# Optimization experiments

Hardware: AMD Instinct MI355X
Metric: run time of the kernel (lower is better)

## Reference

```python
import jax, jax.numpy as jnp
import numpy as np

DIM = 256
HEADS = 4
DH = 64
B, N, H, W, G = 1, 6, 64, 64, 8
QLEN = H * W
SCALE = DH ** -0.5
EPS = 1e-5


def _ln(x, g, b):
    m = x.mean(-1, keepdims=True)
    v = ((x - m) ** 2).mean(-1, keepdims=True)
    return (x - m) / jnp.sqrt(v + EPS) * g + b


def setup_inputs() -> dict:
    key = jax.random.key(0)
    ks = jax.random.split(key, 16)
    hd = HEADS * DH
    p = lambda k, shp: 0.02 * jax.random.normal(k, shp, dtype=jnp.float32)
    inp = {
        'q': jax.random.normal(ks[0], (B, N, DIM, H, W), dtype=jnp.float32),
        'k': jax.random.normal(ks[1], (B, N, QLEN, G, DIM), dtype=jnp.float32),
        'v': jax.random.normal(ks[2], (B, N, QLEN, G, DIM), dtype=jnp.float32),
        'skip': jax.random.normal(ks[3], (B, DIM, H, W), dtype=jnp.float32),
        'mask': jax.random.randint(ks[4], (B, N, QLEN, 1), 0, 2).astype(bool),
        'ln_q_g': jnp.ones((DIM,), jnp.float32), 'ln_q_b': jnp.zeros((DIM,), jnp.float32),
        'wq': p(ks[5], (DIM, hd)), 'bq': jnp.zeros((hd,), jnp.float32),
        'ln_k_g': jnp.ones((DIM,), jnp.float32), 'ln_k_b': jnp.zeros((DIM,), jnp.float32),
        'wk': p(ks[6], (DIM, hd)), 'bk': jnp.zeros((hd,), jnp.float32),
        'ln_v_g': jnp.ones((DIM,), jnp.float32), 'ln_v_b': jnp.zeros((DIM,), jnp.float32),
        'wv': p(ks[7], (DIM, hd)), 'bv': jnp.zeros((hd,), jnp.float32),
        'w_proj': p(ks[8], (hd, DIM)), 'b_proj': jnp.zeros((DIM,), jnp.float32),
        'ln_pre_g': jnp.ones((DIM,), jnp.float32), 'ln_pre_b': jnp.zeros((DIM,), jnp.float32),
        'w_mlp1': p(ks[9], (DIM, 2 * DIM)), 'b_mlp1': jnp.zeros((2 * DIM,), jnp.float32),
        'w_mlp2': p(ks[10], (2 * DIM, DIM)), 'b_mlp2': jnp.zeros((DIM,), jnp.float32),
        'ln_post_g': jnp.ones((DIM,), jnp.float32), 'ln_post_b': jnp.zeros((DIM,), jnp.float32),
    }
    return inp


def reference(q, k, v, skip, mask,
              ln_q_g, ln_q_b, wq, bq,
              ln_k_g, ln_k_b, wk, bk,
              ln_v_g, ln_v_b, wv, bv,
              w_proj, b_proj,
              ln_pre_g, ln_pre_b,
              w_mlp1, b_mlp1, w_mlp2, b_mlp2,
              ln_post_g, ln_post_b):
    b, n, d, Hh, Ww = q.shape
    g = k.shape[-2]
    Qn = Hh * Ww
    # b n d H W -> b n (H W) d
    qx = jnp.transpose(q, (0, 1, 3, 4, 2)).reshape(b, n, Qn, d)
    qp = _ln(qx, ln_q_g, ln_q_b) @ wq + bq            # (b, n, Q, m*dh)
    kp = _ln(k, ln_k_g, ln_k_b) @ wk + bk             # (b, n, Q, g, m*dh)
    vp = _ln(v, ln_v_g, ln_v_b) @ wv + bv             # (b, n, Q, g, m*dh)
    qh = qp.reshape(b, n, Qn, HEADS, DH)
    kh = kp.reshape(b, n, Qn, g, HEADS, DH)
    # scores: (b, m, Q, n, g)
    dot = SCALE * jnp.einsum('bnqmd,bnqgmd->bmqng', qh, kh)
    mb = jnp.transpose(mask[..., 0], (0, 2, 1))[:, None, :, :, None]  # (b,1,Q,n,1)
    dot = jnp.where(mb, dot, jnp.float32(-1e9))
    att = jax.nn.softmax(dot.reshape(b, HEADS, Qn, n * g), axis=-1)
    vh = vp.reshape(b, n, Qn, g, HEADS, DH)
    vh = jnp.transpose(vh, (0, 4, 2, 1, 3, 5)).reshape(b, HEADS, Qn, n * g, DH)
    a = jnp.einsum('bmqk,bmqkd->bmqd', att, vh)       # (b, m, Q, dh)
    a = jnp.transpose(a, (0, 2, 1, 3)).reshape(b, Qn, HEADS * DH)
    z = a @ w_proj + b_proj
    z = z + jnp.transpose(skip, (0, 2, 3, 1)).reshape(b, Qn, d)
    z = _ln(z, ln_pre_g, ln_pre_b)
    h = jax.nn.gelu(z @ w_mlp1 + b_mlp1, approximate=False) @ w_mlp2 + b_mlp2
    z = _ln(z + h, ln_post_g, ln_post_b)
    return jnp.transpose(z.reshape(b, Hh, Ww, d), (0, 3, 1, 2))
```

## Files before the change

### kernel.cpp

```cpp
#include <hip/hip_runtime.h>
#include <hip/hip_bf16.h>
#include <math.h>

#define NF 6
#define QL 4096
#define SCALE 0.125f
#define EPSLN 1e-5f

typedef __bf16 bf16x8 __attribute__((ext_vector_type(8)));
typedef __bf16 bf16x4 __attribute__((ext_vector_type(4)));
typedef float  f32x4  __attribute__((ext_vector_type(4)));

#define OFF_WQT   0u
#define OFF_WKT   131072u
#define OFF_WVT   262144u
#define OFF_WPT   393216u
#define OFF_W1T   524288u
#define OFF_W2T   786432u
#define OFF_QH    1048576u
#define OFF_ATT   13631488u
#define OFF_OPART 16777216u

__device__ __forceinline__ unsigned short f2bf(float x) {
  union { float f; unsigned u; } v; v.f = x;
  unsigned r = v.u + 0x7FFFu + ((v.u >> 16) & 1u);
  return (unsigned short)(r >> 16);
}
__device__ __forceinline__ unsigned long long pack4bf(float a, float b, float c, float d) {
  unsigned d0 = (unsigned)f2bf(a) | ((unsigned)f2bf(b) << 16);
  unsigned d1 = (unsigned)f2bf(c) | ((unsigned)f2bf(d) << 16);
  return (unsigned long long)d0 | ((unsigned long long)d1 << 32);
}

__global__ void __launch_bounds__(256)
prep_kernel(const float* __restrict__ wq, const float* __restrict__ wk,
            const float* __restrict__ wv, const float* __restrict__ wp,
            const float* __restrict__ w1, const float* __restrict__ w2,
            unsigned short* __restrict__ wsu16)
{
  const int blk = blockIdx.x, t = threadIdx.x;
  const float* src; unsigned short* dst; int N, KT, ntile;
  if (blk < 64) {
    int mi = blk >> 4; ntile = blk & 15; N = 256; KT = 8;
    src = (mi == 0) ? wq : (mi == 1) ? wk : (mi == 2) ? wv : wp;
    dst = wsu16 + (size_t)mi * 65536;
  } else if (blk < 96) {
    ntile = blk - 64; N = 512; KT = 8; src = w1; dst = wsu16 + OFF_W1T / 2;
  } else {
    ntile = blk - 96; N = 256; KT = 16; src = w2; dst = wsu16 + OFF_W2T / 2;
  }
  const int lane = t & 63;
  const int lr = lane & 15, quad = lane >> 4;
  const int ncol = ntile * 16 + lr;
  for (int kt = (t >> 6); kt < KT; kt += 4) {
    unsigned v8[8];
#pragma unroll
    for (int j = 0; j < 8; ++j) {
      int krow = kt * 32 + quad * 8 + j;
      v8[j] = f2bf(src[(size_t)krow * N + ncol]);
    }
    uint4 u;
    u.x = v8[0] | (v8[1] << 16); u.y = v8[2] | (v8[3] << 16);
    u.z = v8[4] | (v8[5] << 16); u.w = v8[6] | (v8[7] << 16);
    *(uint4*)(dst + ((size_t)(ntile * KT + kt) * 512 + lane * 8)) = u;
  }
}

__global__ void __launch_bounds__(256, 4)
projq_kernel(const float* __restrict__ src,
             const float* __restrict__ lng, const float* __restrict__ lnb,
             const unsigned short* __restrict__ wTp,
             const float* __restrict__ bias,
             unsigned short* __restrict__ qh)
{
  __shared__ __align__(16) unsigned short s_x[64 * 264];
  const int t = threadIdx.x, blk = blockIdx.x;
  const int n = blk >> 6, qp0 = (blk & 63) << 6;

  {
    const int l16 = t & 15, dg = t >> 4;
    for (int it = 0; it < 16; ++it) {
      int dcol = it * 16 + dg;
      float4 x = *(const float4*)(src + ((size_t)(n * 256 + dcol)) * 4096 + qp0 + l16 * 4);
      s_x[(l16 * 4 + 0) * 264 + dcol] = f2bf(x.x);
      s_x[(l16 * 4 + 1) * 264 + dcol] = f2bf(x.y);
      s_x[(l16 * 4 + 2) * 264 + dcol] = f2bf(x.z);
      s_x[(l16 * 4 + 3) * 264 + dcol] = f2bf(x.w);
    }
  }
  __syncthreads();
  {
    const int row = t >> 2, sl = t & 3;
    float s = 0.f, s2 = 0.f;
#pragma unroll
    for (int i = 0; i < 8; ++i) {
      bf16x8 xv = *(const bf16x8*)(s_x + row * 264 + (i * 4 + sl) * 8);
#pragma unroll
      for (int j = 0; j < 8; ++j) { float f = (float)xv[j]; s += f; s2 += f * f; }
    }
    s += __shfl_xor(s, 1, 64);  s += __shfl_xor(s, 2, 64);
    s2 += __shfl_xor(s2, 1, 64); s2 += __shfl_xor(s2, 2, 64);
    float mu = s * (1.f / 256.f);
    float var = s2 * (1.f / 256.f) - mu * mu;
    float istd = rsqrtf(var + EPSLN);
#pragma unroll
    for (int i = 0; i < 8; ++i) {
      int c = (i * 4 + sl) * 8;
      bf16x8 xv = *(const bf16x8*)(s_x + row * 264 + c);
      f32x4 ga = *(const f32x4*)(lng + c), gb = *(const f32x4*)(lng + c + 4);
      f32x4 ba = *(const f32x4*)(lnb + c), bb = *(const f32x4*)(lnb + c + 4);
      uint4 u;
      u.x = (unsigned)f2bf(((float)xv[0] - mu) * istd * ga[0] + ba[0]) |
            ((unsigned)f2bf(((float)xv[1] - mu) * istd * ga[1] + ba[1]) << 16);
      u.y = (unsigned)f2bf(((float)xv[2] - mu) * istd * ga[2] + ba[2]) |
            ((unsigned)f2bf(((float)xv[3] - mu) * istd * ga[3] + ba[3]) << 16);
      u.z = (unsigned)f2bf(((float)xv[4] - mu) * istd * gb[0] + bb[0]) |
            ((unsigned)f2bf(((float)xv[5] - mu) * istd * gb[1] + bb[1]) << 16);
      u.w = (unsigned)f2bf(((float)xv[6] - mu) * istd * gb[2] + bb[2]) |
            ((unsigned)f2bf(((float)xv[7] - mu) * istd * gb[3] + bb[3]) << 16);
      *(uint4*)(s_x + row * 264 + c) = u;
    }
  }
  __syncthreads();

  const int w = t >> 6, lane = t & 63, lr = lane & 15, quad = lane >> 4;
  f32x4 acc[4][4];
  {
    f32x4 z = {0.f, 0.f, 0.f, 0.f};
#pragma unroll
    for (int a = 0; a < 4; ++a)
#pragma unroll
      for (int b = 0; b < 4; ++b) acc[a][b] = z;
  }
  for (int kt = 0; kt < 8; ++kt) {
    bf16x8 xf[4];
#pragma unroll
    for (int mt = 0; mt < 4; ++mt)
      xf[mt] = *(const bf16x8*)(s_x + (mt * 16 + lr) * 264 + kt * 32 + quad * 8);
#pragma unroll
    for (int nt = 0; nt < 4; ++nt) {
      bf16x8 wf = *(const bf16x8*)(wTp + ((size_t)((w * 4 + nt) * 8 + kt) * 512 + lane * 8));
#pragma unroll
      for (int mt = 0; mt < 4; ++mt)
        acc[nt][mt] = __builtin_amdgcn_mfma_f32_16x16x32_bf16(wf, xf[mt], acc[nt][mt], 0, 0, 0);
    }
  }
  __syncthreads();
#pragma unroll
  for (int nt = 0; nt < 4; ++nt) {
    int n0 = w * 64 + nt * 16 + quad * 4;
    f32x4 bb = *(const f32x4*)(bias + n0);
#pragma unroll
    for (int mt = 0; mt < 4; ++mt) {
      int m = mt * 16 + lr;
      f32x4 a = acc[nt][mt];
      *(unsigned long long*)(s_x + m * 264 + n0) =
          pack4bf(a[0] + bb[0], a[1] + bb[1], a[2] + bb[2], a[3] + bb[3]);
    }
  }
  __syncthreads();
  unsigned char* ob = (unsigned char*)qh + ((size_t)n * QL + qp0) * 512;
#pragma unroll
  for (int i = 0; i < 8; ++i) {
    int lin = i * 4096 + t * 16;
    int r = lin >> 9, off = lin & 511;
    *(uint4*)(ob + lin) = *(const uint4*)((const unsigned char*)s_x + r * 528 + off);
  }
}

__global__ void __launch_bounds__(256, 4)
projkv_kernel(const float* __restrict__ src,
              const float* __restrict__ lng, const float* __restrict__ lnb,
              const unsigned short* __restrict__ wTp,
              const float* __restrict__ bias,
              const unsigned short* __restrict__ qh,
              float* __restrict__ attg,
              const int* __restrict__ mask,
              float* __restrict__ opart,
              int kind)
{
  __shared__ __align__(16) unsigned short s_x[32 * 264];
  __shared__ __align__(16) float s_att[16 * 48];
  const int t = threadIdx.x, blk = blockIdx.x;
  const int n = blk >> 10, qp0 = (blk & 1023) << 2;
  const int w = t >> 6, lane = t & 63;

  {
    const int row = t >> 3, sl = t & 7;
    const float* gr = src + ((size_t)blk * 32 + row) * 256 + sl * 4;
    f32x4 xv[8];
    float s = 0.f, s2 = 0.f;
#pragma unroll
    for (int i = 0; i < 8; ++i) {
      xv[i] = *(const f32x4*)(gr + i * 32);
#pragma unroll
      for (int j = 0; j < 4; ++j) { float f = xv[i][j]; s += f; s2 += f * f; }
    }
    s += __shfl_xor(s, 1, 64);  s += __shfl_xor(s, 2, 64);  s += __shfl_xor(s, 4, 64);
    s2 += __shfl_xor(s2, 1, 64); s2 += __shfl_xor(s2, 2, 64); s2 += __shfl_xor(s2, 4, 64);
    float mu = s * (1.f / 256.f);
    float var = s2 * (1.f / 256.f) - mu * mu;
    float istd = rsqrtf(var + EPSLN);
#pragma unroll
    for (int i = 0; i < 8; ++i) {
      int c = sl * 4 + i * 32;
      f32x4 g = *(const f32x4*)(lng + c);
      f32x4 b = *(const f32x4*)(lnb + c);
      *(unsigned long long*)(s_x + row * 264 + c) =
          pack4bf((xv[i][0] - mu) * istd * g[0] + b[0],
                  (xv[i][1] - mu) * istd * g[1] + b[1],
                  (xv[i][2] - mu) * istd * g[2] + b[2],
                  (xv[i][3] - mu) * istd * g[3] + b[3]);
    }
  }

  if (kind == 1 && t < 64) {
    const int r = t >> 2, sl = t & 3;
    const int p = r >> 2, pix = qp0 + p;
    const float* ar = attg + (((size_t)pix) * 4 + (r & 3)) * 48 + sl * 12;
    float x[12];
#pragma unroll
    for (int i = 0; i < 3; ++i) {
      f32x4 v4 = *(const f32x4*)(ar + i * 4);
      x[i * 4] = v4[0]; x[i * 4 + 1] = v4[1]; x[i * 4 + 2] = v4[2]; x[i * 4 + 3] = v4[3];
    }
#pragma unroll
    for (int i = 0; i < 12; ++i) {
      int nn = (sl * 12 + i) >> 3;
      if (!mask[nn * QL + pix]) x[i] = -1e9f;
    }
    float mx = -3.0e38f;
#pragma unroll
    for (int i = 0; i < 12; ++i) mx = fmaxf(mx, x[i]);
    mx = fmaxf(mx, __shfl_xor(mx, 1, 64));
    mx = fmaxf(mx, __shfl_xor(mx, 2, 64));
    float sm = 0.f;
#pragma unroll
    for (int i = 0; i < 12; ++i) { float e = __expf(x[i] - mx); x[i] = e; sm += e; }
    sm += __shfl_xor(sm, 1, 64);
    sm += __shfl_xor(sm, 2, 64);
    float inv = 1.f / sm;
#pragma unroll
    for (int i = 0; i < 12; ++i) s_att[r * 48 + sl * 12 + i] = x[i] * inv;
  }
  __syncthreads();

  const int lr = lane & 15, quad = lane >> 4;
  f32x4 acc[4][2];
  {
    f32x4 z = {0.f, 0.f, 0.f, 0.f};
#pragma unroll
    for (int a = 0; a < 4; ++a) { acc[a][0] = z; acc[a][1] = z; }
  }
  for (int kt = 0; kt < 8; ++kt) {
    bf16x8 xf[2];
    xf[0] = *(const bf16x8*)(s_x + lr * 264 + kt * 32 + quad * 8);
    xf[1] = *(const bf16x8*)(s_x + (16 + lr) * 264 + kt * 32 + quad * 8);
#pragma unroll
    for (int nt = 0; nt < 4; ++nt) {
      bf16x8 wf = *(const bf16x8*)(wTp + ((size_t)((w * 4 + nt) * 8 + kt) * 512 + lane * 8));
      acc[nt][0] = __builtin_amdgcn_mfma_f32_16x16x32_bf16(wf, xf[0], acc[nt][0], 0, 0, 0);
      acc[nt][1] = __builtin_amdgcn_mfma_f32_16x16x32_bf16(wf, xf[1], acc[nt][1], 0, 0, 0);
    }
  }
  __syncthreads();
#pragma unroll
  for (int nt = 0; nt < 4; ++nt) {
    int n0 = w * 64 + nt * 16 + quad * 4;
    f32x4 bb = *(const f32x4*)(bias + n0);
#pragma unroll
    for (int mt = 0; mt < 2; ++mt) {
      int m = mt * 16 + lr;
      f32x4 a = acc[nt][mt];
      *(unsigned long long*)(s_x + m * 264 + n0) =
          pack4bf(a[0] + bb[0], a[1] + bb[1], a[2] + bb[2], a[3] + bb[3]);
    }
  }
  __syncthreads();

  if (kind == 0) {
    const int p = t >> 6, m = (t >> 4) & 3, g = (t >> 1) & 7, h = t & 1;
    const unsigned short* kr = s_x + (p * 8 + g) * 264 + m * 64 + h * 32;
    const unsigned short* qr = qh + ((size_t)n * QL + qp0 + p) * 256 + m * 64 + h * 32;
    float dot = 0.f;
#pragma unroll
    for (int i = 0; i < 4; ++i) {
      bf16x8 kv = *(const bf16x8*)(kr + i * 8);
      bf16x8 qv = *(const bf16x8*)(qr + i * 8);
#pragma unroll
      for (int j = 0; j < 8; ++j) dot += (float)kv[j] * (float)qv[j];
    }
    dot += __shfl_xor(dot, 1, 64);
    if (h == 0)
      attg[(((size_t)(qp0 + p)) * 4 + m) * 48 + n * 8 + g] = dot * SCALE;
  } else {
    const int p = t >> 6, c0 = (t & 63) * 4, m = c0 >> 6;
    const float* ar = s_att + (p * 4 + m) * 48 + n * 8;
    float aw[8];
#pragma unroll
    for (int j = 0; j < 8; ++j) aw[j] = ar[j];
    float o[4] = {0.f, 0.f, 0.f, 0.f};
#pragma unroll
    for (int g = 0; g < 8; ++g) {
      bf16x4 vv = *(const bf16x4*)(s_x + (p * 8 + g) * 264 + c0);
#pragma unroll
      for (int j = 0; j < 4; ++j) o[j] += aw[g] * (float)vv[j];
    }
    f32x4 ov = {o[0], o[1], o[2], o[3]};
    *(f32x4*)(opart + ((size_t)n * QL + qp0 + p) * 256 + c0) = ov;
  }
}

__global__ void __launch_bounds__(256)
epi_kernel(const float* __restrict__ opart, const float* __restrict__ skip,
           const unsigned short* __restrict__ wpp, const float* __restrict__ bp,
           const float* __restrict__ lng1, const float* __restrict__ lnb1,
           const unsigned short* __restrict__ w1p, const float* __restrict__ b1,
           const unsigned short* __restrict__ w2p, const float* __restrict__ b2,
           const float* __restrict__ lng2, const float* __restrict__ lnb2,
           float* __restrict__ out)
{
  __shared__ __align__(16) unsigned char smem[50688];
  unsigned short* s_a  = (unsigned short*)smem;
  float*          s_z  = (float*)(smem + 8448);
  unsigned short* s_zb = (unsigned short*)(smem + 25344);
  unsigned short* s_h  = (unsigned short*)(smem + 33792);
  float*          s_z2 = (float*)(smem + 33792);
  const int t = threadIdx.x, q0 = blockIdx.x * 16;

#pragma unroll
  for (int i = 0; i < 4; ++i) {
    int pos = i * 256 + t, p = pos >> 6, c4 = (pos & 63) * 4;
    const float* base = opart + (size_t)(q0 + p) * 256 + c4;
    f32x4 s = {0.f, 0.f, 0.f, 0.f};
#pragma unroll
    for (int nn = 0; nn < 6; ++nn) s += *(const f32x4*)(base + (size_t)nn * QL * 256);
    *(unsigned long long*)(s_a + p * 264 + c4) = pack4bf(s[0], s[1], s[2], s[3]);
  }
  __syncthreads();

  const int w = t >> 6, lane = t & 63, lr = lane & 15, quad = lane >> 4;

  {
    f32x4 acc[4];
    f32x4 z = {0.f, 0.f, 0.f, 0.f};
#pragma unroll
    for (int a = 0; a < 4; ++a) acc[a] = z;
    for (int kt = 0; kt < 8; ++kt) {
      bf16x8 xf = *(const bf16x8*)(s_a + lr * 264 + kt * 32 + quad * 8);
#pragma unroll
      for (int nt = 0; nt < 4; ++nt) {
        bf16x8 wf = *(const bf16x8*)(wpp + ((size_t)((w * 4 + nt) * 8 + kt) * 512 + lane * 8));
        acc[nt] = __builtin_amdgcn_mfma_f32_16x16x32_bf16(wf, xf, acc[nt], 0, 0, 0);
      }
    }
#pragma unroll
    for (int nt = 0; nt < 4; ++nt) {
      int n0 = w * 64 + nt * 16 + quad * 4;
      f32x4 bb = *(const f32x4*)(bp + n0);
      f32x4 sk;
#pragma unroll
      for (int j = 0; j < 4; ++j) sk[j] = skip[(size_t)(n0 + j) * QL + q0 + lr];
      *(f32x4*)(s_z + lr * 264 + n0) = acc[nt] + bb + sk;
    }
  }
  __syncthreads();

  {
    int r = t >> 4, l = t & 15;
    float s = 0.f, s2 = 0.f;
#pragma unroll
    for (int i = 0; i < 16; ++i) {
      float x = s_z[r * 264 + l + 16 * i];
      s += x; s2 += x * x;
    }
    s += __shfl_xor(s, 1, 64); s += __shfl_xor(s, 2, 64);
    s += __shfl_xor(s, 4, 64); s += __shfl_xor(s, 8, 64);
    s2 += __shfl_xor(s2, 1, 64); s2 += __shfl_xor(s2, 2, 64);
    s2 += __shfl_xor(s2, 4, 64); s2 += __shfl_xor(s2, 8, 64);
    float mu = s * (1.f / 256.f);
    float var = s2 * (1.f / 256.f) - mu * mu;
    float istd = rsqrtf(var + EPSLN);
#pragma unroll
    for (int i = 0; i < 16; ++i) {
      int d = l + 16 * i;
      float nv = (s_z[r * 264 + d] - mu) * istd * lng1[d] + lnb1[d];
      s_z[r * 264 + d] = nv;
      s_zb[r * 264 + d] = f2bf(nv);
    }
  }
  __syncthreads();

  {
    f32x4 acc[8];
    f32x4 z = {0.f, 0.f, 0.f, 0.f};
#pragma unroll
    for (int a = 0; a < 8; ++a) acc[a] = z;
    for (int kt = 0; kt < 8; ++kt) {
      bf16x8 xf = *(const bf16x8*)(s_zb + lr * 264 + kt * 32 + quad * 8);
#pragma unroll
      for (int nt = 0; nt < 8; ++nt) {
        bf16x8 wf = *(const bf16x8*)(w1p + ((size_t)((w * 8 + nt) * 8 + kt) * 512 + lane * 8));
        acc[nt] = __builtin_amdgcn_mfma_f32_16x16x32_bf16(wf, xf, acc[nt], 0, 0, 0);
      }
    }
#pragma unroll
    for (int nt = 0; nt < 8; ++nt) {
      int n0 = w * 128 + nt * 16 + quad * 4;
      f32x4 bb = *(const f32x4*)(b1 + n0);
      float hv[4];
#pragma unroll
      for (int j = 0; j < 4; ++j) {
        float val = acc[nt][j] + bb[j];
        hv[j] = 0.5f * val * (1.f + erff(val * 0.70710678118654752f));
      }
      *(unsigned long long*)(s_h + lr * 528 + n0) = pack4bf(hv[0], hv[1], hv[2], hv[3]);
    }
  }
  __syncthreads();

  {
    f32x4 acc[4];
    f32x4 z = {0.f, 0.f, 0.f, 0.f};
#pragma unroll
    for (int a = 0; a < 4; ++a) acc[a] = z;
    for (int kt = 0; kt < 16; ++kt) {
      bf16x8 xf = *(const bf16x8*)(s_h + lr * 528 + kt * 32 + quad * 8);
#pragma unroll
      for (int nt = 0; nt < 4; ++nt) {
        bf16x8 wf = *(const bf16x8*)(w2p + ((size_t)((w * 4 + nt) * 16 + kt) * 512 + lane * 8));
        acc[nt] = __builtin_amdgcn_mfma_f32_16x16x32_bf16(wf, xf, acc[nt], 0, 0, 0);
      }
    }
    f32x4 res[4];
#pragma unroll
    for (int nt = 0; nt < 4; ++nt) {
      int n0 = w * 64 + nt * 16 + quad * 4;
      f32x4 bb = *(const f32x4*)(b2 + n0);
      f32x4 zr = *(const f32x4*)(s_z + lr * 264 + n0);
      res[nt] = acc[nt] + bb + zr;
    }
    __syncthreads();
#pragma unroll
    for (int nt = 0; nt < 4; ++nt) {
      int n0 = w * 64 + nt * 16 + quad * 4;
      *(f32x4*)(s_z2 + lr * 264 + n0) = res[nt];
    }
  }
  __syncthreads();

  {
    int r = t >> 4, l = t & 15;
    float s = 0.f, s2 = 0.f;
#pragma unroll
    for (int i = 0; i < 16; ++i) {
      float x = s_z2[r * 264 + l + 16 * i];
      s += x; s2 += x * x;
    }
    s += __shfl_xor(s, 1, 64); s += __shfl_xor(s, 2, 64);
    s += __shfl_xor(s, 4, 64); s += __shfl_xor(s, 8, 64);
    s2 += __shfl_xor(s2, 1, 64); s2 += __shfl_xor(s2, 2, 64);
    s2 += __shfl_xor(s2, 4, 64); s2 += __shfl_xor(s2, 8, 64);
    float mu = s * (1.f / 256.f);
    float var = s2 * (1.f / 256.f) - mu * mu;
    float istd = rsqrtf(var + EPSLN);
#pragma unroll
    for (int i = 0; i < 16; ++i) {
      int d = l + 16 * i;
      s_z2[r * 264 + d] = (s_z2[r * 264 + d] - mu) * istd * lng2[d] + lnb2[d];
    }
  }
  __syncthreads();

#pragma unroll
  for (int i = 0; i < 16; ++i) {
    int c = i * 16 + (t >> 4), p = t & 15;
    out[(size_t)c * QL + q0 + p] = s_z2[p * 264 + c];
  }
}

extern "C" void kernel_launch(void* const* d_in, const int* in_sizes, int n_in,
                              void* d_out, int out_size, void* d_ws, size_t ws_size,
                              hipStream_t stream) {
  (void)in_sizes; (void)n_in; (void)out_size; (void)ws_size;
  const float* q     = (const float*)d_in[0];
  const float* k     = (const float*)d_in[1];
  const float* v     = (const float*)d_in[2];
  const float* skip  = (const float*)d_in[3];
  const int*   mask  = (const int*)d_in[4];
  const float* lnqg  = (const float*)d_in[5];
  const float* lnqb  = (const float*)d_in[6];
  const float* wq    = (const float*)d_in[7];
  const float* bq    = (const float*)d_in[8];
  const float* lnkg  = (const float*)d_in[9];
  const float* lnkb  = (const float*)d_in[10];
  const float* wk    = (const float*)d_in[11];
  const float* bk    = (const float*)d_in[12];
  const float* lnvg  = (const float*)d_in[13];
  const float* lnvb  = (const float*)d_in[14];
  const float* wv    = (const float*)d_in[15];
  const float* bv    = (const float*)d_in[16];
  const float* wp    = (const float*)d_in[17];
  const float* bp    = (const float*)d_in[18];
  const float* lng1  = (const float*)d_in[19];
  const float* lnb1  = (const float*)d_in[20];
  const float* w1    = (const float*)d_in[21];
  const float* b1    = (const float*)d_in[22];
  const float* w2    = (const float*)d_in[23];
  const float* b2    = (const float*)d_in[24];
  const float* lng2  = (const float*)d_in[25];
  const float* lnb2  = (const float*)d_in[26];
  float* out = (float*)d_out;

  unsigned char* ws = (unsigned char*)d_ws;
  unsigned short* wsu16 = (unsigned short*)d_ws;
  unsigned short* wqT = (unsigned short*)(ws + OFF_WQT);
  unsigned short* wkT = (unsigned short*)(ws + OFF_WKT);
  unsigned short* wvT = (unsigned short*)(ws + OFF_WVT);
  unsigned short* wpT = (unsigned short*)(ws + OFF_WPT);
  unsigned short* w1T = (unsigned short*)(ws + OFF_W1T);
  unsigned short* w2T = (unsigned short*)(ws + OFF_W2T);
  unsigned short* qh  = (unsigned short*)(ws + OFF_QH);
  float* attg  = (float*)(ws + OFF_ATT);
  float* opart = (float*)(ws + OFF_OPART);

  hipLaunchKernelGGL(prep_kernel, dim3(112), dim3(256), 0, stream,
                     wq, wk, wv, wp, w1, w2, wsu16);
  hipLaunchKernelGGL(projq_kernel, dim3(384), dim3(256), 0, stream,
                     q, lnqg, lnqb, wqT, bq, qh);
  hipLaunchKernelGGL(projkv_kernel, dim3(6144), dim3(256), 0, stream,
                     k, lnkg, lnkb, wkT, bk, qh, attg, mask, opart, 0);
  hipLaunchKernelGGL(projkv_kernel, dim3(6144), dim3(256), 0, stream,
                     v, lnvg, lnvb, wvT, bv, qh, attg, mask, opart, 1);
  hipLaunchKernelGGL(epi_kernel, dim3(QL / 16), dim3(256), 0, stream,
                     opart, skip, wpT, bp, lng1, lnb1, w1T, b1, w2T, b2, lng2, lnb2, out);
}
```

Baseline: 555.7 us.

## Fuse K and V projection, softmax and weighted sum into one per-pixel kernel

Replaces the two separate K and V projection launches with one kernel per query pixel. Each block stages the K rows for all six cameras, computes scores, applies mask and softmax, then stages V and produces the weighted sum in shared memory. This removes the global round trips of the score buffer and the six partial-output buffers (about 25 MB of fp32 opart writes and reads), and the epilogue now reads a single reduced attention output. In exchange, K and V loads are serialised inside each block. The per-block tile is also reorganised around 48 rows with strided gathers across cameras.

```diff
diff --git a/kernel.cpp b/kernel.cpp
--- a/kernel.cpp
+++ b/kernel.cpp
@@ -19,7 +19,6 @@
 #define OFF_W2T   786432u
 #define OFF_QH    1048576u
 #define OFF_ATT   13631488u
-#define OFF_OPART 16777216u
 
 __device__ __forceinline__ unsigned short f2bf(float x) {
   union { float f; unsigned u; } v; v.f = x;
@@ -168,26 +167,16 @@
   }
 }
 
-__global__ void __launch_bounds__(256, 4)
-projkv_kernel(const float* __restrict__ src,
-              const float* __restrict__ lng, const float* __restrict__ lnb,
-              const unsigned short* __restrict__ wTp,
-              const float* __restrict__ bias,
-              const unsigned short* __restrict__ qh,
-              float* __restrict__ attg,
-              const int* __restrict__ mask,
-              float* __restrict__ opart,
-              int kind)
+__device__ __forceinline__ void stage_ln_rows(
+    const float* __restrict__ src, int p, int row0, int nrows,
+    const float* __restrict__ lng, const float* __restrict__ lnb,
+    unsigned short* __restrict__ s_x, int t)
 {
-  __shared__ __align__(16) unsigned short s_x[32 * 264];
-  __shared__ __align__(16) float s_att[16 * 48];
-  const int t = threadIdx.x, blk = blockIdx.x;
-  const int n = blk >> 10, qp0 = (blk & 1023) << 2;
-  const int w = t >> 6, lane = t & 63;
-
-  {
-    const int row = t >> 3, sl = t & 7;
-    const float* gr = src + ((size_t)blk * 32 + row) * 256 + sl * 4;
+  const int rel = t >> 3;
+  if (rel < nrows) {
+    const int row = row0 + rel, sl = t & 7;
+    const int n = row >> 3, g = row & 7;
+    const float* gr = src + ((size_t)((n * 4096 + p) * 8 + g)) * 256 + sl * 4;
     f32x4 xv[8];
     float s = 0.f, s2 = 0.f;
 #pragma unroll
@@ -204,115 +193,186 @@
 #pragma unroll
     for (int i = 0; i < 8; ++i) {
       int c = sl * 4 + i * 32;
-      f32x4 g = *(const f32x4*)(lng + c);
-      f32x4 b = *(const f32x4*)(lnb + c);
+      f32x4 g4 = *(const f32x4*)(lng + c);
+      f32x4 b4 = *(const f32x4*)(lnb + c);
       *(unsigned long long*)(s_x + row * 264 + c) =
-          pack4bf((xv[i][0] - mu) * istd * g[0] + b[0],
-                  (xv[i][1] - mu) * istd * g[1] + b[1],
-                  (xv[i][2] - mu) * istd * g[2] + b[2],
-                  (xv[i][3] - mu) * istd * g[3] + b[3]);
-    }
-  }
-
-  if (kind == 1 && t < 64) {
+          pack4bf((xv[i][0] - mu) * istd * g4[0] + b4[0],
+                  (xv[i][1] - mu) * istd * g4[1] + b4[1],
+                  (xv[i][2] - mu) * istd * g4[2] + b4[2],
+                  (xv[i][3] - mu) * istd * g4[3] + b4[3]);
+    }
+  }
+}
+
+__global__ void __launch_bounds__(256, 4)
+fused_attn_kernel(const float* __restrict__ ksrc, const float* __restrict__ vsrc,
+                  const float* __restrict__ lnkg, const float* __restrict__ lnkb,
+                  const unsigned short* __restrict__ wkT, const float* __restrict__ bk,
+                  const float* __restrict__ lnvg, const float* __restrict__ lnvb,
+                  const unsigned short* __restrict__ wvT, const float* __restrict__ bv,
+                  const unsigned short* __restrict__ qh,
+                  const int* __restrict__ mask,
+                  float* __restrict__ att_out)
+{
+  __shared__ __align__(16) unsigned short s_x[48 * 264];
+  __shared__ __align__(16) unsigned short s_q[6 * 264];
+  __shared__ __align__(16) float s_att[4 * 48];
+  const int t = threadIdx.x, p = blockIdx.x;
+  const int w = t >> 6, lane = t & 63, lr = lane & 15, quad = lane >> 4;
+
+  if (t < 192) {
+    int n = t >> 5, c8 = (t & 31) * 8;
+    *(uint4*)(s_q + n * 264 + c8) = *(const uint4*)(qh + ((size_t)(n * QL + p)) * 256 + c8);
+  }
+  stage_ln_rows(ksrc, p, 0, 32, lnkg, lnkb, s_x, t);
+  stage_ln_rows(ksrc, p, 32, 16, lnkg, lnkb, s_x, t);
+  __syncthreads();
+
+  {
+    f32x4 acc[4][3];
+    {
+      f32x4 z = {0.f, 0.f, 0.f, 0.f};
+#pragma unroll
+      for (int a = 0; a < 4; ++a)
+#pragma unroll
+        for (int b = 0; b < 3; ++b) acc[a][b] = z;
+    }
+    for (int kt = 0; kt < 8; ++kt) {
+      bf16x8 xf[3];
+#pragma unroll
+      for (int mt = 0; mt < 3; ++mt)
+        xf[mt] = *(const bf16x8*)(s_x + (mt * 16 + lr) * 264 + kt * 32 + quad * 8);
+#pragma unroll
+      for (int nt = 0; nt < 4; ++nt) {
+        bf16x8 wf = *(const bf16x8*)(wkT + ((size_t)((w * 4 + nt) * 8 + kt) * 512 + lane * 8));
+#pragma unroll
+        for (int mt = 0; mt < 3; ++mt)
+          acc[nt][mt] = __builtin_amdgcn_mfma_f32_16x16x32_bf16(wf, xf[mt], acc[nt][mt], 0, 0, 0);
+      }
+    }
+    __syncthreads();
+#pragma unroll
+    for (int nt = 0; nt < 4; ++nt) {
+      int n0 = w * 64 + nt * 16 + quad * 4;
+      f32x4 bb = *(const f32x4*)(bk + n0);
+#pragma unroll
+      for (int mt = 0; mt < 3; ++mt) {
+        int m = mt * 16 + lr;
+        f32x4 a = acc[nt][mt];
+        *(unsigned long long*)(s_x + m * 264 + n0) =
+            pack4bf(a[0] + bb[0], a[1] + bb[1], a[2] + bb[2], a[3] + bb[3]);
+      }
+    }
+  }
+  __syncthreads();
+
+  if (t < 192) {
+    const int m = t / 48, key = t % 48;
+    const unsigned short* kr = s_x + key * 264 + m * 64;
+    const unsigned short* qr = s_q + (key >> 3) * 264 + m * 64;
+    float dot = 0.f;
+#pragma unroll
+    for (int i = 0; i < 8; ++i) {
+      bf16x8 kv = *(const bf16x8*)(kr + i * 8);
+      bf16x8 qv = *(const bf16x8*)(qr + i * 8);
+#pragma unroll
+      for (int j = 0; j < 8; ++j) dot += (float)kv[j] * (float)qv[j];
+    }
+    s_att[m * 48 + key] = dot * SCALE;
+  }
+  __syncthreads();
+
+  stage_ln_rows(vsrc, p, 0, 32, lnvg, lnvb, s_x, t);
+  stage_ln_rows(vsrc, p, 32, 16, lnvg, lnvb, s_x, t);
+  if (t < 16) {
     const int r = t >> 2, sl = t & 3;
-    const int p = r >> 2, pix = qp0 + p;
-    const float* ar = attg + (((size_t)pix) * 4 + (r & 3)) * 48 + sl * 12;
     float x[12];
 #pragma unroll
-    for (int i = 0; i < 3; ++i) {
-      f32x4 v4 = *(const f32x4*)(ar + i * 4);
-      x[i * 4] = v4[0]; x[i * 4 + 1] = v4[1]; x[i * 4 + 2] = v4[2]; x[i * 4 + 3] = v4[3];
-    }
-#pragma unroll
-    for (int i = 0; i < 12; ++i) {
-      int nn = (sl * 12 + i) >> 3;
-      if (!mask[nn * QL + pix]) x[i] = -1e9f;
+    for (int j = 0; j < 12; ++j) {
+      int key = sl * 12 + j;
+      float v = s_att[r * 48 + key];
+      x[j] = mask[(key >> 3) * QL + p] ? v : -1e9f;
     }
     float mx = -3.0e38f;
 #pragma unroll
-    for (int i = 0; i < 12; ++i) mx = fmaxf(mx, x[i]);
+    for (int j = 0; j < 12; ++j) mx = fmaxf(mx, x[j]);
     mx = fmaxf(mx, __shfl_xor(mx, 1, 64));
     mx = fmaxf(mx, __shfl_xor(mx, 2, 64));
     float sm = 0.f;
 #pragma unroll
-    for (int i = 0; i < 12; ++i) { float e = __expf(x[i] - mx); x[i] = e; sm += e; }
+    for (int j = 0; j < 12; ++j) { float e = __expf(x[j] - mx); x[j] = e; sm += e; }
     sm += __shfl_xor(sm, 1, 64);
     sm += __shfl_xor(sm, 2, 64);
     float inv = 1.f / sm;
 #pragma unroll
-    for (int i = 0; i < 12; ++i) s_att[r * 48 + sl * 12 + i] = x[i] * inv;
-  }
-  __syncthreads();
-
-  const int lr = lane & 15, quad = lane >> 4;
-  f32x4 acc[4][2];
-  {
-    f32x4 z = {0.f, 0.f, 0.f, 0.f};
-#pragma unroll
-    for (int a = 0; a < 4; ++a) { acc[a][0] = z; acc[a][1] = z; }
-  }
-  for (int kt = 0; kt < 8; ++kt) {
-    bf16x8 xf[2];
-    xf[0] = *(const bf16x8*)(s_x + lr * 264 + kt * 32 + quad * 8);
-    xf[1] = *(const bf16x8*)(s_x + (16 + lr) * 264 + kt * 32 + quad * 8);
+    for (int j = 0; j < 12; ++j) s_att[r * 48 + sl * 12 + j] = x[j] * inv;
+  }
+  __syncthreads();
+
+  {
+    f32x4 acc[4][3];
+    {
+      f32x4 z = {0.f, 0.f, 0.f, 0.f};
+#pragma unroll
+      for (int a = 0; a < 4; ++a)
+#pragma unroll
+        for (int b = 0; b < 3; ++b) acc[a][b] = z;
+    }
+    for (int kt = 0; kt < 8; ++kt) {
+      bf16x8 xf[3];
+#pragma unroll
+      for (int mt = 0; mt < 3; ++mt)
+        xf[mt] = *(const bf16x8*)(s_x + (mt * 16 + lr) * 264 + kt * 32 + quad * 8);
+#pragma unroll
+      for (int nt = 0; nt < 4; ++nt) {
+        bf16x8 wf = *(const bf16x8*)(wvT + ((size_t)((w * 4 + nt) * 8 + kt) * 512 + lane * 8));
+#pragma unroll
+        for (int mt = 0; mt < 3; ++mt)
+          acc[nt][mt] = __builtin_amdgcn_mfma_f32_16x16x32_bf16(wf, xf[mt], acc[nt][mt], 0, 0, 0);
+      }
+    }
+    __syncthreads();
 #pragma unroll
     for (int nt = 0; nt < 4; ++nt) {
-      bf16x8 wf = *(const bf16x8*)(wTp + ((size_t)((w * 4 + nt) * 8 + kt) * 512 + lane * 8));
-      acc[nt][0] = __builtin_amdgcn_mfma_f32_16x16x32_bf16(wf, xf[0], acc[nt][0], 0, 0, 0);
-      acc[nt][1] = __builtin_amdgcn_mfma_f32_16x16x32_bf16(wf, xf[1], acc[nt][1], 0, 0, 0);
-    }
-  }
-  __syncthreads();
-#pragma unroll
-  for (int nt = 0; nt < 4; ++nt) {
-    int n0 = w * 64 + nt * 16 + quad * 4;
-    f32x4 bb = *(const f32x4*)(bias + n0);
-#pragma unroll
-    for (int mt = 0; mt < 2; ++mt) {
-      int m = mt * 16 + lr;
-      f32x4 a = acc[nt][mt];
-      *(unsigned long long*)(s_x + m * 264 + n0) =
-          pack4bf(a[0] + bb[0], a[1] + bb[1], a[2] + bb[2], a[3] + bb[3]);
-    }
-  }
-  __syncthreads();
-
-  if (kind == 0) {
-    const int p = t >> 6, m = (t >> 4) & 3, g = (t >> 1) & 7, h = t & 1;
-    const unsigned short* kr = s_x + (p * 8 + g) * 264 + m * 64 + h * 32;
-    const unsigned short* qr = qh + ((size_t)n * QL + qp0 + p) * 256 + m * 64 + h * 32;
-    float dot = 0.f;
-#pragma unroll
-    for (int i = 0; i < 4; ++i) {
-      bf16x8 kv = *(const bf16x8*)(kr + i * 8);
-      bf16x8 qv = *(const bf16x8*)(qr + i * 8);
-#pragma unroll
-      for (int j = 0; j < 8; ++j) dot += (float)kv[j] * (float)qv[j];
-    }
-    dot += __shfl_xor(dot, 1, 64);
-    if (h == 0)
-      attg[(((size_t)(qp0 + p)) * 4 + m) * 48 + n * 8 + g] = dot * SCALE;
-  } else {
-    const int p = t >> 6, c0 = (t & 63) * 4, m = c0 >> 6;
-    const float* ar = s_att + (p * 4 + m) * 48 + n * 8;
-    float aw[8];
-#pragma unroll
-    for (int j = 0; j < 8; ++j) aw[j] = ar[j];
+      int n0 = w * 64 + nt * 16 + quad * 4;
+      f32x4 bb = *(const f32x4*)(bv + n0);
+#pragma unroll
+      for (int mt = 0; mt < 3; ++mt) {
+        int m = mt * 16 + lr;
+        f32x4 a = acc[nt][mt];
+        *(unsigned long long*)(s_x + m * 264 + n0) =
+            pack4bf(a[0] + bb[0], a[1] + bb[1], a[2] + bb[2], a[3] + bb[3]);
+      }
+    }
+  }
+  __syncthreads();
+
+  {
+    const int cq = t >> 2, ks = t & 3, m = cq >> 4;
+    float aw[12];
+#pragma unroll
+    for (int j = 0; j < 12; ++j) aw[j] = s_att[m * 48 + ks * 12 + j];
     float o[4] = {0.f, 0.f, 0.f, 0.f};
 #pragma unroll
-    for (int g = 0; g < 8; ++g) {
-      bf16x4 vv = *(const bf16x4*)(s_x + (p * 8 + g) * 264 + c0);
-#pragma unroll
-      for (int j = 0; j < 4; ++j) o[j] += aw[g] * (float)vv[j];
-    }
-    f32x4 ov = {o[0], o[1], o[2], o[3]};
-    *(f32x4*)(opart + ((size_t)n * QL + qp0 + p) * 256 + c0) = ov;
+    for (int j = 0; j < 12; ++j) {
+      bf16x4 vv = *(const bf16x4*)(s_x + (ks * 12 + j) * 264 + cq * 4);
+#pragma unroll
+      for (int c = 0; c < 4; ++c) o[c] += aw[j] * (float)vv[c];
+    }
+#pragma unroll
+    for (int c = 0; c < 4; ++c) {
+      o[c] += __shfl_xor(o[c], 1, 64);
+      o[c] += __shfl_xor(o[c], 2, 64);
+    }
+    if (ks == 0) {
+      f32x4 ov = {o[0], o[1], o[2], o[3]};
+      *(f32x4*)(att_out + (size_t)p * 256 + cq * 4) = ov;
+    }
   }
 }
 
 __global__ void __launch_bounds__(256)
-epi_kernel(const float* __restrict__ opart, const float* __restrict__ skip,
+epi_kernel(const float* __restrict__ att_in, const float* __restrict__ skip,
            const unsigned short* __restrict__ wpp, const float* __restrict__ bp,
            const float* __restrict__ lng1, const float* __restrict__ lnb1,
            const unsigned short* __restrict__ w1p, const float* __restrict__ b1,
@@ -331,10 +391,7 @@
 #pragma unroll
   for (int i = 0; i < 4; ++i) {
     int pos = i * 256 + t, p = pos >> 6, c4 = (pos & 63) * 4;
-    const float* base = opart + (size_t)(q0 + p) * 256 + c4;
-    f32x4 s = {0.f, 0.f, 0.f, 0.f};
-#pragma unroll
-    for (int nn = 0; nn < 6; ++nn) s += *(const f32x4*)(base + (size_t)nn * QL * 256);
+    f32x4 s = *(const f32x4*)(att_in + (size_t)(q0 + p) * 256 + c4);
     *(unsigned long long*)(s_a + p * 264 + c4) = pack4bf(s[0], s[1], s[2], s[3]);
   }
   __syncthreads();
@@ -521,17 +578,14 @@
   unsigned short* w1T = (unsigned short*)(ws + OFF_W1T);
   unsigned short* w2T = (unsigned short*)(ws + OFF_W2T);
   unsigned short* qh  = (unsigned short*)(ws + OFF_QH);
-  float* attg  = (float*)(ws + OFF_ATT);
-  float* opart = (float*)(ws + OFF_OPART);
+  float* att_out = (float*)(ws + OFF_ATT);
 
   hipLaunchKernelGGL(prep_kernel, dim3(112), dim3(256), 0, stream,
                      wq, wk, wv, wp, w1, w2, wsu16);
   hipLaunchKernelGGL(projq_kernel, dim3(384), dim3(256), 0, stream,
                      q, lnqg, lnqb, wqT, bq, qh);
-  hipLaunchKernelGGL(projkv_kernel, dim3(6144), dim3(256), 0, stream,
-                     k, lnkg, lnkb, wkT, bk, qh, attg, mask, opart, 0);
-  hipLaunchKernelGGL(projkv_kernel, dim3(6144), dim3(256), 0, stream,
-                     v, lnvg, lnvb, wvT, bv, qh, attg, mask, opart, 1);
+  hipLaunchKernelGGL(fused_attn_kernel, dim3(QL), dim3(256), 0, stream,
+                     k, v, lnkg, lnkb, wkT, bk, lnvg, lnvb, wvT, bv, qh, mask, att_out);
   hipLaunchKernelGGL(epi_kernel, dim3(QL / 16), dim3(256), 0, stream,
-                     opart, skip, wpT, bp, lng1, lnb1, w1T, b1, w2T, b2, lng2, lnb2, out);
-}
+                     att_out, skip, wpT, bp, lng1, lnb1, w1T, b1, w2T, b2, lng2, lnb2, out);
+}
```

New measurement: 550.6 us. No clear change (-0.9%).
